# Kernel tuning notes

Measured on AMD Instinct MI355X. Metric: run time of the kernel, lower is better.

Reference implementation:

```python
import jax, jax.numpy as jnp
import numpy as np

B, T, C, D = 16, 2048, 1024, 128  # batch, seq, n_embd, head_size

def setup_inputs() -> dict:
    key = jax.random.key(0)
    kx, kq, kk, kv = jax.random.split(key, 4)
    x = jax.random.normal(kx, (B, T, C), dtype=jnp.float32)
    s = 1.0 / np.sqrt(C)
    Wq = jax.random.normal(kq, (C, D), dtype=jnp.float32) * s
    Wk = jax.random.normal(kk, (C, D), dtype=jnp.float32) * s
    Wv = jax.random.normal(kv, (C, D), dtype=jnp.float32) * s
    return {"x": x, "Wq": Wq, "Wk": Wk, "Wv": Wv}

def reference(x, Wq, Wk, Wv):
    # q,k,v: [B,T,D]
    q = jnp.einsum('btc,cd->btd', x, Wq)
    k = jnp.einsum('btc,cd->btd', x, Wk)
    v = jnp.einsum('btc,cd->btd', x, Wv)
    scale = 1.0 / jnp.sqrt(jnp.asarray(q.shape[-1], q.dtype))
    wei = jnp.einsum('bqd,bkd->bqk', q, k) * scale  # [B,T,T]
    causal = jnp.tril(jnp.ones((T, T), dtype=bool))
    wei = jnp.where(causal, wei, -jnp.inf)
    wei = jax.nn.softmax(wei, axis=-1)
    # dropout is identity in eval mode
    out = jnp.einsum('bqk,bkd->bqd', wei, v)  # [B,T,D]
    return out
```

## Files before the change

### kernel.cpp

```cpp
#include <hip/hip_runtime.h>

typedef unsigned short u16;
typedef unsigned int   u32;
typedef __attribute__((ext_vector_type(8)))  __bf16 bf16x8;
typedef __attribute__((ext_vector_type(16))) float  f32x16;
typedef __attribute__((ext_vector_type(4)))  float  fl4;
typedef __attribute__((ext_vector_type(4)))  u16    u16x4;
typedef __attribute__((ext_vector_type(4)))  u32    u32x4;

#define NB 16
#define NT 2048
#define NC 1024
#define ND 128


__device__ __forceinline__ u16 f2bf(float f) {
  u32 u = __builtin_bit_cast(u32, f);
  u = (u + 0x7fffu + ((u >> 16) & 1u)) >> 16;
  return (u16)u;
}

__device__ __forceinline__ u32 pk2(float lo, float hi) {
  return (u32)f2bf(lo) | ((u32)f2bf(hi) << 16);
}

__device__ __forceinline__ void gll16(const u16* g, u16* l) {
  __builtin_amdgcn_global_load_lds(
      (const __attribute__((address_space(1))) void*)g,
      (__attribute__((address_space(3))) void*)l, 16, 0, 0);
}

__global__ __launch_bounds__(256) void wprep_k(
    const float* __restrict__ Wq, const float* __restrict__ Wk,
    const float* __restrict__ Wv, u16* __restrict__ wf)
{
  const int cb   = blockIdx.x;
  const int kind = cb >> 2;
  const float* __restrict__ W = (kind == 0) ? Wq : (kind == 1) ? Wk : Wv;
  const int lane = threadIdx.x & 63;
  const int ksq  = threadIdx.x >> 6;
  const int l31 = lane & 31, hi = lane >> 5;
  const int d = (cb & 3) * 32 + l31;
  u16* __restrict__ o = wf + (size_t)cb * 64 * 512;
  #pragma unroll 4
  for (int ii = 0; ii < 16; ++ii) {
    int ks = ksq * 16 + ii;
    int k  = ks * 16 + hi * 8;
    u16x4 p0, p1;
    #pragma unroll
    for (int j = 0; j < 4; ++j) p0[j] = f2bf(W[(size_t)(k + j) * ND + d]);
    #pragma unroll
    for (int j = 0; j < 4; ++j) p1[j] = f2bf(W[(size_t)(k + 4 + j) * ND + d]);
    u16* dst = o + ((size_t)ks * 64 + lane) * 8;
    *(u16x4*)dst = p0;
    *(u16x4*)(dst + 4) = p1;
  }
}

__global__ __launch_bounds__(128, 4) void qkv_fused_k(
    const float* __restrict__ x, const u16* __restrict__ wf,
    u16* __restrict__ qf, u16* __restrict__ kf, u16* __restrict__ vf)
{
  const int L   = blockIdx.x;
  const int rt  = L & 511;
  const int cq  = L >> 9;
  const int tid = threadIdx.x;
  const int lane = tid & 63;
  const int wid  = tid >> 6;
  const int l31 = lane & 31, hi = lane >> 5;

  __shared__ u16 As[64 * 64];
  __shared__ u16 Bs[12 * 512];

  const int arow = tid >> 4;
  const int ac4  = (tid & 15) * 4;
  const float* __restrict__ xr = x + ((size_t)rt * 64 + arow) * NC + ac4;

  fl4 pA[8];
  auto issueA = [&](int k0) {
    #pragma unroll
    for (int i = 0; i < 8; ++i)
      pA[i] = *(const fl4*)(xr + (size_t)i * 8 * NC + k0);
  };
  auto writeA = [&]() {
    char* b = (char*)As;
    #pragma unroll
    for (int i = 0; i < 8; ++i) {
      int row = i * 8 + arow;
      u16x4 pk;
      pk[0] = f2bf(pA[i][0]); pk[1] = f2bf(pA[i][1]);
      pk[2] = f2bf(pA[i][2]); pk[3] = f2bf(pA[i][3]);
      *(u16x4*)(b + row * 128 + ((ac4 * 2) ^ ((row & 7) << 4))) = pk;
    }
  };

  const u16* __restrict__ wfb = wf + (size_t)(cq * 3) * 64 * 512;

  f32x16 acc[3] = {};

  issueA(0);
  for (int k = 0; k < 16; ++k) {
    __syncthreads();
    #pragma unroll
    for (int j = 0; j < 6; ++j) {
      int c = wid * 6 + j;
      gll16(wfb + (((size_t)(c >> 2) * 64 + k * 4 + (c & 3)) * 64 + lane) * 8,
            &Bs[c * 512]);
    }
    writeA();
    __syncthreads();
    if (k < 15) issueA((k + 1) * 64);
    const char* ab = (const char*)As;
    #pragma unroll
    for (int ks = 0; ks < 4; ++ks) {
      int row = wid * 32 + l31;
      bf16x8 a = *(const bf16x8*)(ab + row * 128 + ((ks * 32 + hi * 16) ^ ((row & 7) << 4)));
      #pragma unroll
      for (int cb = 0; cb < 3; ++cb) {
        bf16x8 b = *(const bf16x8*)&Bs[(cb * 4 + ks) * 512 + lane * 8];
        acc[cb] = __builtin_amdgcn_mfma_f32_32x32x16_bf16(a, b, acc[cb], 0, 0, 0);
      }
    }
  }

  const int t32 = rt * 2 + wid;
  #pragma unroll
  for (int cb = 0; cb < 3; ++cb) {
    const int colb = cq * 96 + cb * 32;
    const int kind = colb >> 7;
    const int d    = (colb & 127) + l31;
    if (kind < 2) {
      u16* __restrict__ o = kind ? kf : qf;
      const float sc = kind ? 1.0f : 0.12752539240377073f;
      const int ds = d >> 4, b3 = (d >> 3) & 1, j = d & 7;
      u16* __restrict__ base = o + ((size_t)t32 * 8 + ds) * 512 + 32 * b3 * 8 + j;
      #pragma unroll
      for (int r = 0; r < 16; ++r) {
        int crow = (r & 3) + 8 * (r >> 2) + 4 * hi;
        base[crow * 8] = f2bf(acc[cb][r] * sc);
      }
    } else {
      const int dt = (d & 127) >> 5;
      #pragma unroll
      for (int g = 0; g < 4; ++g) {
        int c16   = t32 * 2 + (g >> 1);
        int lanep = l31 + 32 * (g & 1);
        u16x4 pk;
        #pragma unroll
        for (int jj = 0; jj < 4; ++jj) pk[jj] = f2bf(acc[cb][g * 4 + jj]);
        *(u16x4*)(vf + (((size_t)c16 * 4 + dt) * 64 + lanep) * 8 + 4 * hi) = pk;
      }
    }
  }
}

__global__ __launch_bounds__(128, 2) void attn_fwd_k(
    const u16* __restrict__ qw, const u16* __restrict__ kw,
    const u16* __restrict__ vw, float* __restrict__ out)
{
  const int tid  = threadIdx.x;
  const int lane = tid & 63;
  const int w    = tid >> 6;
  const int l31  = lane & 31;
  const int hi   = lane >> 5;

  const int c  = blockIdx.x;
  const int bb = (c >> 6) & 15;
  const int qi = ((c & 63) + ((c >> 8) << 4)) & 63;
  const int q0 = qi * 32;
  const int qrow = q0 + l31;

  const u16* __restrict__ qb = qw + ((size_t)bb * 64 + qi) * 4096;
  const u16* __restrict__ kb = kw + (size_t)bb * 64 * 4096;
  const u16* __restrict__ vb = vw + (size_t)bb * 128 * 2048;

  __shared__ float ofs[64][64];
  __shared__ float mls[2][64];

  bf16x8 qfr[8];
  #pragma unroll
  for (int s = 0; s < 8; ++s)
    qfr[s] = *(const bf16x8*)(qb + ((size_t)s * 64 + lane) * 8);

  f32x16 of[4] = {};
  float m_run = -__builtin_inff();
  float l_run = 0.f;

  const int nsteps = (qi >> 1) + 1;
  for (int s = w; s < nsteps; s += 2) {
    const int kv0 = s * 64;
    const bool masked = (s == nsteps - 1);

    bf16x8 kf0[8], kf1[8];
    #pragma unroll
    for (int t = 0; t < 8; ++t) {
      kf0[t] = *(const bf16x8*)(kb + (((size_t)(2 * s) * 8 + t) * 64 + lane) * 8);
      kf1[t] = *(const bf16x8*)(kb + (((size_t)(2 * s + 1) * 8 + t) * 64 + lane) * 8);
    }
    f32x16 st0 = {}, st1 = {};
    #pragma unroll
    for (int t = 0; t < 8; ++t) {
      st0 = __builtin_amdgcn_mfma_f32_32x32x16_bf16(kf0[t], qfr[t], st0, 0, 0, 0);
      st1 = __builtin_amdgcn_mfma_f32_32x32x16_bf16(kf1[t], qfr[t], st1, 0, 0, 0);
    }
    bf16x8 vfr[4][4];
    #pragma unroll
    for (int ks = 0; ks < 4; ++ks)
      #pragma unroll
      for (int dt = 0; dt < 4; ++dt)
        vfr[dt][ks] = *(const bf16x8*)(vb + (((size_t)((kv0 >> 4) + ks) * 4 + dt) * 64 + lane) * 8);

    if (masked) {
      #pragma unroll
      for (int r = 0; r < 16; ++r) {
        int crow = (r & 3) + 8 * (r >> 2) + 4 * hi;
        st0[r] = (kv0 + crow      <= qrow) ? st0[r] : -1e30f;
        st1[r] = (kv0 + 32 + crow <= qrow) ? st1[r] : -1e30f;
      }
    }

    float pmax = -1e30f;
    #pragma unroll
    for (int r = 0; r < 16; ++r) pmax = fmaxf(pmax, fmaxf(st0[r], st1[r]));
    pmax = fmaxf(pmax, __shfl_xor(pmax, 32, 64));

    const bool no_rescale = (pmax <= m_run);
    const float m_new = fmaxf(m_run, pmax);
    const float fac = __builtin_amdgcn_exp2f(m_run - m_new);
    float rsum = 0.f;
    #pragma unroll
    for (int r = 0; r < 16; ++r) {
      st0[r] = __builtin_amdgcn_exp2f(st0[r] - m_new);
      st1[r] = __builtin_amdgcn_exp2f(st1[r] - m_new);
      rsum += st0[r] + st1[r];
    }
    rsum += __shfl_xor(rsum, 32, 64);
    l_run = l_run * fac + rsum;
    m_run = m_new;

    if (!__all(no_rescale)) {
      #pragma unroll
      for (int r = 0; r < 16; ++r) {
        float fr = __shfl(fac, (r & 3) + 8 * (r >> 2) + 4 * hi, 64);
        #pragma unroll
        for (int dt = 0; dt < 4; ++dt) of[dt][r] *= fr;
      }
    }

    u32x4 pa[4];
    #pragma unroll
    for (int g = 0; g < 4; ++g) {
      const float* sp = (g < 2) ? (const float*)&st0 : (const float*)&st1;
      const int o8 = (g & 1) * 8;
      u32 a0 = pk2(sp[o8 + 0], sp[o8 + 1]);
      u32 a1 = pk2(sp[o8 + 2], sp[o8 + 3]);
      u32 b0 = pk2(sp[o8 + 4], sp[o8 + 5]);
      u32 b1 = pk2(sp[o8 + 6], sp[o8 + 7]);
      u32 ta0 = __shfl_xor(a0, 32, 64);
      u32 ta1 = __shfl_xor(a1, 32, 64);
      u32 tb0 = __shfl_xor(b0, 32, 64);
      u32 tb1 = __shfl_xor(b1, 32, 64);
      pa[g][0] = hi ? tb0 : a0;
      pa[g][1] = hi ? tb1 : a1;
      pa[g][2] = hi ? b0  : ta0;
      pa[g][3] = hi ? b1  : ta1;
    }

    #pragma unroll
    for (int ks = 0; ks < 4; ++ks) {
      bf16x8 paf = __builtin_bit_cast(bf16x8, pa[ks]);
      #pragma unroll
      for (int dt = 0; dt < 4; ++dt)
        of[dt] = __builtin_amdgcn_mfma_f32_32x32x16_bf16(paf, vfr[dt][ks], of[dt], 0, 0, 0);
    }
  }

  if (w == 1) {
    #pragma unroll
    for (int dt = 0; dt < 4; ++dt)
      #pragma unroll
      for (int r = 0; r < 16; ++r)
        ofs[dt * 16 + r][lane] = of[dt][r];
    mls[0][lane] = m_run;
    mls[1][lane] = l_run;
  }
  __syncthreads();
  if (w == 0) {
    const float m1 = mls[0][l31];
    const float l1 = mls[1][l31];
    const float mt = fmaxf(m_run, m1);
    const float f0 = __builtin_amdgcn_exp2f(m_run - mt);
    const float f1 = __builtin_amdgcn_exp2f(m1 - mt);
    const float lt = l_run * f0 + l1 * f1;
    const float rl = 1.0f / lt;
    #pragma unroll
    for (int r = 0; r < 16; ++r) {
      int crow = (r & 3) + 8 * (r >> 2) + 4 * hi;
      float f0r = __shfl(f0, crow, 64);
      float f1r = __shfl(f1, crow, 64);
      float lr  = __shfl(rl, crow, 64);
      #pragma unroll
      for (int dt = 0; dt < 4; ++dt)
        out[((size_t)(bb * NT + q0 + crow)) * ND + dt * 32 + l31] =
            (of[dt][r] * f0r + ofs[dt * 16 + r][lane] * f1r) * lr;
    }
  }
}

extern "C" void kernel_launch(void* const* d_in, const int* in_sizes, int n_in,
                              void* d_out, int out_size, void* d_ws, size_t ws_size,
                              hipStream_t stream) {
  (void)in_sizes; (void)n_in; (void)out_size; (void)ws_size;
  const float* x  = (const float*)d_in[0];
  const float* Wq = (const float*)d_in[1];
  const float* Wk = (const float*)d_in[2];
  const float* Wv = (const float*)d_in[3];
  float* out = (float*)d_out;

  u16* qws = (u16*)d_ws;
  u16* kws = qws + (size_t)NB * NT * ND;
  u16* vws = kws + (size_t)NB * NT * ND;
  u16* wfs = vws + (size_t)NB * NT * ND;

  wprep_k<<<dim3(12), dim3(256), 0, stream>>>(Wq, Wk, Wv, wfs);
  qkv_fused_k<<<dim3(2048), dim3(128), 0, stream>>>(x, wfs, qws, kws, vws);
  attn_fwd_k<<<dim3(1024), dim3(128), 0, stream>>>(qws, kws, vws, out);
}
```

Before: 112.6 us.

## Restructure QKV projection into single-wave blocks with x-tile L2 reuse

The QKV projection kernel now runs 64-thread blocks, each covering 32 rows. Block indices are reordered so the four column-quarter blocks that read the same x rows are launched next to each other, which should let x be served from L2 instead of being fetched from HBM four times. The weight tiles are read straight from global memory into registers rather than staged in LDS with global_load_lds. The x tile is double-buffered in LDS with no barriers, since only one wave touches it. In exchange the kernel issues more global loads for the weights and runs twice as many smaller blocks.

```diff
diff --git a/kernel.cpp b/kernel.cpp
--- a/kernel.cpp
+++ b/kernel.cpp
@@ -22,12 +22,6 @@
 
 __device__ __forceinline__ u32 pk2(float lo, float hi) {
   return (u32)f2bf(lo) | ((u32)f2bf(hi) << 16);
-}
-
-__device__ __forceinline__ void gll16(const u16* g, u16* l) {
-  __builtin_amdgcn_global_load_lds(
-      (const __attribute__((address_space(1))) void*)g,
-      (__attribute__((address_space(3))) void*)l, 16, 0, 0);
 }
 
 __global__ __launch_bounds__(256) void wprep_k(
@@ -57,36 +51,33 @@
   }
 }
 
-__global__ __launch_bounds__(128, 4) void qkv_fused_k(
+__global__ __launch_bounds__(64, 4) void qkv_fused_k(
     const float* __restrict__ x, const u16* __restrict__ wf,
     u16* __restrict__ qf, u16* __restrict__ kf, u16* __restrict__ vf)
 {
-  const int L   = blockIdx.x;
-  const int rt  = L & 511;
-  const int cq  = L >> 9;
+  const int L  = blockIdx.x;
+  const int cq = L & 3;
+  const int rt = L >> 2;
   const int tid = threadIdx.x;
-  const int lane = tid & 63;
-  const int wid  = tid >> 6;
-  const int l31 = lane & 31, hi = lane >> 5;
-
-  __shared__ u16 As[64 * 64];
-  __shared__ u16 Bs[12 * 512];
+  const int l31 = tid & 31, hi = tid >> 5;
+
+  __shared__ u16 As[2][32 * 64];
 
   const int arow = tid >> 4;
   const int ac4  = (tid & 15) * 4;
-  const float* __restrict__ xr = x + ((size_t)rt * 64 + arow) * NC + ac4;
+  const float* __restrict__ xr = x + ((size_t)rt * 32 + arow) * NC + ac4;
 
   fl4 pA[8];
   auto issueA = [&](int k0) {
     #pragma unroll
     for (int i = 0; i < 8; ++i)
-      pA[i] = *(const fl4*)(xr + (size_t)i * 8 * NC + k0);
+      pA[i] = *(const fl4*)(xr + (size_t)i * 4 * NC + k0);
   };
-  auto writeA = [&]() {
-    char* b = (char*)As;
+  auto writeA = [&](u16* dstbuf) {
+    char* b = (char*)dstbuf;
     #pragma unroll
     for (int i = 0; i < 8; ++i) {
-      int row = i * 8 + arow;
+      int row = i * 4 + arow;
       u16x4 pk;
       pk[0] = f2bf(pA[i][0]); pk[1] = f2bf(pA[i][1]);
       pk[2] = f2bf(pA[i][2]); pk[3] = f2bf(pA[i][3]);
@@ -94,36 +85,34 @@
     }
   };
 
-  const u16* __restrict__ wfb = wf + (size_t)(cq * 3) * 64 * 512;
+  const u16* __restrict__ wfb = wf + (size_t)(cq * 3) * 64 * 512 + (size_t)tid * 8;
 
   f32x16 acc[3] = {};
 
   issueA(0);
+  writeA(As[0]);
+  issueA(64);
+
+  #pragma unroll 2
   for (int k = 0; k < 16; ++k) {
-    __syncthreads();
-    #pragma unroll
-    for (int j = 0; j < 6; ++j) {
-      int c = wid * 6 + j;
-      gll16(wfb + (((size_t)(c >> 2) * 64 + k * 4 + (c & 3)) * 64 + lane) * 8,
-            &Bs[c * 512]);
-    }
-    writeA();
-    __syncthreads();
-    if (k < 15) issueA((k + 1) * 64);
-    const char* ab = (const char*)As;
+    const int cur = k & 1;
+    const char* ab = (const char*)As[cur];
     #pragma unroll
     for (int ks = 0; ks < 4; ++ks) {
-      int row = wid * 32 + l31;
-      bf16x8 a = *(const bf16x8*)(ab + row * 128 + ((ks * 32 + hi * 16) ^ ((row & 7) << 4)));
+      bf16x8 a = *(const bf16x8*)(ab + l31 * 128 + ((ks * 32 + hi * 16) ^ ((l31 & 7) << 4)));
       #pragma unroll
       for (int cb = 0; cb < 3; ++cb) {
-        bf16x8 b = *(const bf16x8*)&Bs[(cb * 4 + ks) * 512 + lane * 8];
+        bf16x8 b = *(const bf16x8*)(wfb + ((size_t)cb * 64 + k * 4 + ks) * 512);
         acc[cb] = __builtin_amdgcn_mfma_f32_32x32x16_bf16(a, b, acc[cb], 0, 0, 0);
       }
     }
-  }
-
-  const int t32 = rt * 2 + wid;
+    if (k < 15) {
+      writeA(As[cur ^ 1]);
+      if (k < 14) issueA((k + 2) * 64);
+    }
+  }
+
+  const int t32 = rt;
   #pragma unroll
   for (int cb = 0; cb < 3; ++cb) {
     const int colb = cq * 96 + cb * 32;
@@ -323,6 +312,6 @@
   u16* wfs = vws + (size_t)NB * NT * ND;
 
   wprep_k<<<dim3(12), dim3(256), 0, stream>>>(Wq, Wk, Wv, wfs);
-  qkv_fused_k<<<dim3(2048), dim3(128), 0, stream>>>(x, wfs, qws, kws, vws);
+  qkv_fused_k<<<dim3(4096), dim3(64), 0, stream>>>(x, wfs, qws, kws, vws);
   attn_fwd_k<<<dim3(1024), dim3(128), 0, stream>>>(qws, kws, vws, out);
 }
```

Result: slower. 143.9 us (+27.8%).
